# Optimization experiments

Hardware: AMD Instinct MI355X
Metric: run time of the kernel (lower is better)

The kernel has to match this reference:

```python
import jax, jax.numpy as jnp
import numpy as np

B = 256
V = 6890
J = 24
NUM_BETAS = 10
# standard SMPL kinematic tree
PARENTS = np.array([-1, 0, 0, 0, 1, 2, 3, 4, 5, 6, 7, 8, 9, 9, 9, 12, 13, 14, 16, 17, 18, 19, 20, 21], dtype=np.int64)


def setup_inputs() -> dict:
    key = jax.random.key(0)
    ks = jax.random.split(key, 7)
    betas = jax.random.normal(ks[0], (B, NUM_BETAS), dtype=jnp.float32)
    pose = jax.random.normal(ks[1], (B, J * 3), dtype=jnp.float32) * 0.3
    v_template = jax.random.normal(ks[2], (V, 3), dtype=jnp.float32)
    shapedirs = jax.random.normal(ks[3], (V, 3, NUM_BETAS), dtype=jnp.float32) * 0.01
    posedirs = jax.random.normal(ks[4], ((J - 1) * 9, V * 3), dtype=jnp.float32) * 0.01
    jr = jax.random.uniform(ks[5], (J, V), dtype=jnp.float32)
    J_regressor = jr / jnp.sum(jr, axis=1, keepdims=True)
    # skinning weights per vertex sum to 1
    w = jax.random.uniform(ks[6], (V, J), dtype=jnp.float32)
    lbs_weights = w / jnp.sum(w, axis=1, keepdims=True)
    return {"betas": betas, "pose": pose, "v_template": v_template,
            "shapedirs": shapedirs, "posedirs": posedirs,
            "J_regressor": J_regressor, "lbs_weights": lbs_weights,
            "parents": PARENTS}


def batch_rodrigues(rot_vecs):
    # rot_vecs: (N,3) axis-angle -> (N,3,3)
    angle = jnp.linalg.norm(rot_vecs + 1e-8, axis=1, keepdims=True)  # (N,1)
    rot_dir = rot_vecs / angle
    cos = jnp.cos(angle)[:, :, None]  # (N,1,1)
    sin = jnp.sin(angle)[:, :, None]
    rx, ry, rz = rot_dir[:, 0], rot_dir[:, 1], rot_dir[:, 2]
    z = jnp.zeros_like(rx)
    K = jnp.stack([z, -rz, ry, rz, z, -rx, -ry, rx, z], axis=1).reshape(-1, 3, 3)
    ident = jnp.eye(3, dtype=rot_vecs.dtype)[None]
    return ident + sin * K + (1.0 - cos) * jnp.matmul(K, K)


def batch_rigid_transform(rot_mats, joints, parents):
    # rot_mats: (B,J,3,3), joints: (B,J,3)
    b, n = joints.shape[:2]
    rel_joints = joints.at[:, 1:].add(-joints[:, parents[1:]])
    bottom = jnp.broadcast_to(jnp.array([0., 0., 0., 1.], dtype=joints.dtype), (b, n, 1, 4))
    tm = jnp.concatenate([jnp.concatenate([rot_mats, rel_joints[..., None]], axis=-1), bottom], axis=-2)  # (B,J,4,4)
    chain = [tm[:, 0]]
    for i in range(1, n):  # fixed 24-joint kinematic tree
        chain.append(jnp.matmul(chain[int(parents[i])], tm[:, i]))
    transforms = jnp.stack(chain, axis=1)  # (B,J,4,4)
    posed_joints = transforms[:, :, :3, 3]
    joints_homogen = jnp.concatenate([joints, jnp.zeros((b, n, 1), dtype=joints.dtype)], axis=-1)
    t = jnp.einsum('bnij,bnj->bni', transforms, joints_homogen)  # (B,J,4)
    rel_transforms = transforms.at[:, :, :, 3].add(-t)
    return posed_joints, rel_transforms


def reference(betas, pose, v_template, shapedirs, posedirs, J_regressor, lbs_weights, parents):
    b = betas.shape[0]
    ident = jnp.eye(3, dtype=pose.dtype)
    # shape blend shapes
    v_shaped = v_template[None] + jnp.einsum('bl,vkl->bvk', betas, shapedirs)  # (B,V,3)
    Jts = jnp.einsum('bvk,jv->bjk', v_shaped, J_regressor)  # (B,J,3)
    # axis-angle -> rotmats, append 2 identity hand rotations
    rot = batch_rodrigues(pose[:, :-6].reshape(-1, 3)).reshape(b, -1, 3, 3)
    hand = jnp.broadcast_to(ident, (b, 2, 3, 3))
    rot_mats = jnp.concatenate([rot, hand], axis=1)  # (B,24,3,3)
    # pose blend shapes (root excluded)
    pose_feature = (rot_mats[:, 1:] - ident).reshape(b, -1)  # (B,207)
    pose_offsets = jnp.matmul(pose_feature, posedirs).reshape(b, -1, 3)
    v_posed = pose_offsets + v_shaped
    # kinematic chain
    J_transformed, A = batch_rigid_transform(rot_mats, Jts, parents)
    # linear blend skinning
    T = jnp.einsum('vj,bjmn->bvmn', lbs_weights, A)  # (B,V,4,4)
    v_homo = jnp.concatenate([v_posed, jnp.ones((b, v_posed.shape[1], 1), dtype=v_posed.dtype)], axis=-1)
    verts = jnp.einsum('bvmn,bvn->bvm', T, v_homo)[..., :3]
    return verts.astype(jnp.float32), J_transformed.astype(jnp.float32)
```

## Files before the change

kernel.cpp:

```cpp
#include <hip/hip_runtime.h>
#include <math.h>

#define B_N 256
#define V_N 6890
#define J_N 24
#define KPF 207
#define KE  218
#define NCOL (V_N*3)

typedef float v2f __attribute__((ext_vector_type(2)));

__device__ __constant__ int c_par[24] = {-1,0,0,0,1,2,3,4,5,6,7,8,9,9,9,12,13,14,16,17,18,19,20,21};

#define WS_PF   0
#define WS_A    (WS_PF + B_N*KE)
#define WS_EXT  (WS_A + B_N*J_N*12)
#define WS_PART (WS_EXT + 11*NCOL)

__global__ __launch_bounds__(256) void k_jreg(const float* __restrict__ Jreg,
        const float* __restrict__ vt, const float* __restrict__ sd,
        float* __restrict__ part)
{
    int j = blockIdx.x;
    int c = blockIdx.y;
    int tid = threadIdx.x;
    int v0 = c * 1723;
    int v1 = v0 + 1723; if (v1 > V_N) v1 = V_N;

    float acc[33];
    #pragma unroll
    for (int i = 0; i < 33; ++i) acc[i] = 0.f;

    for (int v = v0 + tid; v < v1; v += 256) {
        float r = Jreg[j*V_N + v];
        const float* s = sd + v*30;
        #pragma unroll
        for (int i = 0; i < 30; ++i) acc[i] += r * s[i];
        #pragma unroll
        for (int k = 0; k < 3; ++k) acc[30+k] += r * vt[v*3+k];
    }
    #pragma unroll
    for (int i = 0; i < 33; ++i) {
        #pragma unroll
        for (int off = 32; off > 0; off >>= 1)
            acc[i] += __shfl_down(acc[i], off, 64);
    }
    __shared__ float red[4][33];
    int wave = tid >> 6, lane = tid & 63;
    if (lane == 0) {
        #pragma unroll
        for (int i = 0; i < 33; ++i) red[wave][i] = acc[i];
    }
    __syncthreads();
    if (tid < 33) {
        float s = red[0][tid] + red[1][tid] + red[2][tid] + red[3][tid];
        part[(j*4 + c)*33 + tid] = s;
    }
}

__global__ __launch_bounds__(256) void k_ext(const float* __restrict__ sd,
        const float* __restrict__ vt, float* __restrict__ EXT)
{
    int idx = blockIdx.x*256 + threadIdx.x;
    if (idx >= NCOL) return;
    int v = idx / 3, k = idx - v*3;
    #pragma unroll
    for (int l = 0; l < 10; ++l) EXT[l*NCOL + idx] = sd[v*30 + k*10 + l];
    EXT[10*NCOL + idx] = vt[idx];
}

__global__ __launch_bounds__(64) void k_batch(const float* __restrict__ pose,
        const float* __restrict__ betas, const float* __restrict__ part,
        float* __restrict__ PFt, float* __restrict__ A, float* __restrict__ outJ)
{
    int b = blockIdx.x;
    int lane = threadIdx.x;
    __shared__ float sR[24][9];
    __shared__ float sJ[24][3];
    __shared__ float sG[24][12];

    if (lane < 24) {
        float R[9];
        if (lane < 22) {
            float p0 = pose[b*72 + lane*3 + 0];
            float p1 = pose[b*72 + lane*3 + 1];
            float p2 = pose[b*72 + lane*3 + 2];
            float a0 = p0 + 1e-8f, a1 = p1 + 1e-8f, a2 = p2 + 1e-8f;
            float angle = sqrtf(a0*a0 + a1*a1 + a2*a2);
            float inv = 1.f / angle;
            float rx = p0*inv, ry = p1*inv, rz = p2*inv;
            float cc = cosf(angle), ss = sinf(angle), ic = 1.f - cc;
            R[0] = 1.f - ic*(ry*ry + rz*rz);
            R[1] = -ss*rz + ic*rx*ry;
            R[2] =  ss*ry + ic*rx*rz;
            R[3] =  ss*rz + ic*rx*ry;
            R[4] = 1.f - ic*(rx*rx + rz*rz);
            R[5] = -ss*rx + ic*ry*rz;
            R[6] = -ss*ry + ic*rx*rz;
            R[7] =  ss*rx + ic*ry*rz;
            R[8] = 1.f - ic*(rx*rx + ry*ry);
        } else {
            R[0]=1.f;R[1]=0.f;R[2]=0.f;R[3]=0.f;R[4]=1.f;R[5]=0.f;R[6]=0.f;R[7]=0.f;R[8]=1.f;
        }
        #pragma unroll
        for (int e = 0; e < 9; ++e) sR[lane][e] = R[e];
    }
    __syncthreads();
    for (int idx = lane; idx < 72; idx += 64) {
        int j = idx / 3, k = idx - j*3;
        const float* p0 = part + (j*4 + 0)*33;
        const float* p1 = part + (j*4 + 1)*33;
        const float* p2 = part + (j*4 + 2)*33;
        const float* p3 = part + (j*4 + 3)*33;
        float s = p0[30+k] + p1[30+k] + p2[30+k] + p3[30+k];
        #pragma unroll
        for (int l = 0; l < 10; ++l) {
            float js = p0[k*10+l] + p1[k*10+l] + p2[k*10+l] + p3[k*10+l];
            s += betas[b*10+l] * js;
        }
        sJ[j][k] = s;
    }
    __syncthreads();
    for (int idx = lane; idx < KPF; idx += 64) {
        int jj = 1 + idx/9, e = idx - (idx/9)*9;
        float id = (e==0 || e==4 || e==8) ? 1.f : 0.f;
        PFt[idx*B_N + b] = sR[jj][e] - id;
    }
    if (lane < 10) PFt[(KPF+lane)*B_N + b] = betas[b*10 + lane];
    if (lane == 0) PFt[217*B_N + b] = 1.f;

    if (lane == 0) {
        #pragma unroll
        for (int r = 0; r < 3; ++r) {
            sG[0][r*4+0] = sR[0][r*3+0];
            sG[0][r*4+1] = sR[0][r*3+1];
            sG[0][r*4+2] = sR[0][r*3+2];
            sG[0][r*4+3] = sJ[0][r];
        }
        for (int i = 1; i < 24; ++i) {
            int p = c_par[i];
            float rel0 = sJ[i][0]-sJ[p][0], rel1 = sJ[i][1]-sJ[p][1], rel2 = sJ[i][2]-sJ[p][2];
            for (int r = 0; r < 3; ++r) {
                float g0 = sG[p][r*4+0], g1 = sG[p][r*4+1], g2 = sG[p][r*4+2], g3 = sG[p][r*4+3];
                sG[i][r*4+0] = g0*sR[i][0] + g1*sR[i][3] + g2*sR[i][6];
                sG[i][r*4+1] = g0*sR[i][1] + g1*sR[i][4] + g2*sR[i][7];
                sG[i][r*4+2] = g0*sR[i][2] + g1*sR[i][5] + g2*sR[i][8];
                sG[i][r*4+3] = g0*rel0 + g1*rel1 + g2*rel2 + g3;
            }
        }
    }
    __syncthreads();
    if (lane < 24) {
        int i = lane;
        #pragma unroll
        for (int r = 0; r < 3; ++r) {
            float g0 = sG[i][r*4+0], g1 = sG[i][r*4+1], g2 = sG[i][r*4+2], g3 = sG[i][r*4+3];
            outJ[b*72 + i*3 + r] = g3;
            float t = g3 - (g0*sJ[i][0] + g1*sJ[i][1] + g2*sJ[i][2]);
            A[(b*24+i)*12 + r*4+0] = g0;
            A[(b*24+i)*12 + r*4+1] = g1;
            A[(b*24+i)*12 + r*4+2] = g2;
            A[(b*24+i)*12 + r*4+3] = t;
        }
    }
}

__global__ __launch_bounds__(256, 2) void k_fused(
        const float* __restrict__ posedirs, const float* __restrict__ EXT,
        const float* __restrict__ PFt, const float* __restrict__ A,
        const float* __restrict__ W, float* __restrict__ out)
{
    constexpr int BT = 32;
    __shared__ __align__(16) float smem[BT*288];

    int tid  = threadIdx.x;
    int wave = tid >> 6, lane = tid & 63;

    int bid = blockIdx.x;
    int w   = (bid & 7)*108 + (bid >> 3);
    int vt  = w >> 3, bt = w & 7;
    int v0 = vt * 64;
    int b0 = bt * BT;
    int v  = v0 + lane;

    int col = (v < V_N) ? v*3 : v0*3;

    #pragma unroll 1
    for (int idx = tid; idx < KE*BT; idx += 256) {
        int r = idx >> 5, bl = idx & 31;
        smem[r*BT + bl] = PFt[r*B_N + b0 + bl];
    }
    __syncthreads();

    v2f axy[8];
    v2f az[4];
    #pragma unroll
    for (int k = 0; k < 8; ++k) axy[k] = (v2f){0.f, 0.f};
    #pragma unroll
    for (int k = 0; k < 4; ++k) az[k] = (v2f){0.f, 0.f};

    int pfb = wave*8;

#define ROW_BODY                                                                  \
    {                                                                             \
        float x = p[0], y = p[1], z = p[2];                                       \
        const float4 pa = *reinterpret_cast<const float4*>(&smem[r*BT + pfb]);    \
        const float4 pb = *reinterpret_cast<const float4*>(&smem[r*BT + pfb + 4]);\
        v2f xy = {x, y};                                                          \
        v2f zz = {z, z};                                                          \
        axy[0] = __builtin_elementwise_fma((v2f){pa.x,pa.x}, xy, axy[0]);         \
        axy[1] = __builtin_elementwise_fma((v2f){pa.y,pa.y}, xy, axy[1]);         \
        axy[2] = __builtin_elementwise_fma((v2f){pa.z,pa.z}, xy, axy[2]);         \
        axy[3] = __builtin_elementwise_fma((v2f){pa.w,pa.w}, xy, axy[3]);         \
        axy[4] = __builtin_elementwise_fma((v2f){pb.x,pb.x}, xy, axy[4]);         \
        axy[5] = __builtin_elementwise_fma((v2f){pb.y,pb.y}, xy, axy[5]);         \
        axy[6] = __builtin_elementwise_fma((v2f){pb.z,pb.z}, xy, axy[6]);         \
        axy[7] = __builtin_elementwise_fma((v2f){pb.w,pb.w}, xy, axy[7]);         \
        az[0]  = __builtin_elementwise_fma((v2f){pa.x,pa.y}, zz, az[0]);          \
        az[1]  = __builtin_elementwise_fma((v2f){pa.z,pa.w}, zz, az[1]);          \
        az[2]  = __builtin_elementwise_fma((v2f){pb.x,pb.y}, zz, az[2]);          \
        az[3]  = __builtin_elementwise_fma((v2f){pb.z,pb.w}, zz, az[3]);          \
    }

    {
        const float* p = posedirs + col;
        #pragma unroll 8
        for (int r = 0; r < KPF; ++r) {
            ROW_BODY
            p += NCOL;
        }
    }
    {
        const float* p = EXT + col;
        #pragma unroll
        for (int r = KPF; r < KE; ++r) {
            ROW_BODY
            p += NCOL;
        }
    }
#undef ROW_BODY

    __syncthreads();

    {
        const float* Ag = A + (size_t)b0*288;
        #pragma unroll 1
        for (int idx = tid; idx < BT*288; idx += 256)
            smem[idx] = Ag[idx];
    }

    int vc = (v < V_N) ? v : (V_N - 1);
    const float4* W4 = reinterpret_cast<const float4*>(W + (size_t)vc*24);
    float4 w0 = W4[0], w1 = W4[1], w2 = W4[2], w3 = W4[3], w4 = W4[4], w5 = W4[5];
    __syncthreads();

    float wv[24] = {w0.x,w0.y,w0.z,w0.w, w1.x,w1.y,w1.z,w1.w, w2.x,w2.y,w2.z,w2.w,
                    w3.x,w3.y,w3.z,w3.w, w4.x,w4.y,w4.z,w4.w, w5.x,w5.y,w5.z,w5.w};

    #pragma unroll
    for (int k = 0; k < 8; ++k) {
        int bb = wave*8 + k;
        const float* Ab = smem + bb*288;
        v2f T01 = {0.f,0.f}, T23 = {0.f,0.f}, T45 = {0.f,0.f};
        v2f T67 = {0.f,0.f}, T89 = {0.f,0.f}, Tab = {0.f,0.f};
        #pragma unroll
        for (int j = 0; j < 24; ++j) {
            float ww = wv[j];
            v2f wwv = {ww, ww};
            float4 a0 = *reinterpret_cast<const float4*>(Ab + j*12 + 0);
            float4 a1 = *reinterpret_cast<const float4*>(Ab + j*12 + 4);
            float4 a2 = *reinterpret_cast<const float4*>(Ab + j*12 + 8);
            T01 = __builtin_elementwise_fma(wwv, (v2f){a0.x,a0.y}, T01);
            T23 = __builtin_elementwise_fma(wwv, (v2f){a0.z,a0.w}, T23);
            T45 = __builtin_elementwise_fma(wwv, (v2f){a1.x,a1.y}, T45);
            T67 = __builtin_elementwise_fma(wwv, (v2f){a1.z,a1.w}, T67);
            T89 = __builtin_elementwise_fma(wwv, (v2f){a2.x,a2.y}, T89);
            Tab = __builtin_elementwise_fma(wwv, (v2f){a2.z,a2.w}, Tab);
        }
        if (v < V_N) {
            float x = axy[k].x, y = axy[k].y;
            float z = (k & 1) ? az[k>>1].y : az[k>>1].x;
            size_t o = (size_t)(b0 + bb)*NCOL + (size_t)v*3;
            out[o+0] = T01.x*x + T01.y*y + T23.x*z + T23.y;
            out[o+1] = T45.x*x + T45.y*y + T67.x*z + T67.y;
            out[o+2] = T89.x*x + T89.y*y + Tab.x*z + Tab.y;
        }
    }
}

extern "C" void kernel_launch(void* const* d_in, const int* in_sizes, int n_in,
                              void* d_out, int out_size, void* d_ws, size_t ws_size,
                              hipStream_t stream)
{
    const float* betas      = (const float*)d_in[0];
    const float* pose       = (const float*)d_in[1];
    const float* v_template = (const float*)d_in[2];
    const float* shapedirs  = (const float*)d_in[3];
    const float* posedirs   = (const float*)d_in[4];
    const float* Jreg       = (const float*)d_in[5];
    const float* lbs        = (const float*)d_in[6];

    float* ws   = (float*)d_ws;
    float* PFt  = ws + WS_PF;
    float* A    = ws + WS_A;
    float* EXT  = ws + WS_EXT;
    float* part = ws + WS_PART;

    float* verts = (float*)d_out;
    float* outJ  = verts + (size_t)B_N*V_N*3;

    hipLaunchKernelGGL(k_jreg, dim3(24,4), dim3(256), 0, stream, Jreg, v_template, shapedirs, part);
    hipLaunchKernelGGL(k_ext, dim3((NCOL+255)/256), dim3(256), 0, stream, shapedirs, v_template, EXT);
    hipLaunchKernelGGL(k_batch, dim3(256), dim3(64), 0, stream, pose, betas, part, PFt, A, outJ);
    hipLaunchKernelGGL(k_fused, dim3(8*108), dim3(256), 0, stream, posedirs, EXT, PFt, A, lbs, verts);
}
```

Baseline: 87.41 us.

## Merge preprocessing kernels and halve shared memory in fused skinning kernel

```diff
diff --git a/kernel.cpp b/kernel.cpp
--- a/kernel.cpp
+++ b/kernel.cpp
@@ -17,56 +17,57 @@
 #define WS_EXT  (WS_A + B_N*J_N*12)
 #define WS_PART (WS_EXT + 11*NCOL)
 
-__global__ __launch_bounds__(256) void k_jreg(const float* __restrict__ Jreg,
+__global__ __launch_bounds__(256) void k_pre(const float* __restrict__ Jreg,
         const float* __restrict__ vt, const float* __restrict__ sd,
-        float* __restrict__ part)
+        float* __restrict__ part, float* __restrict__ EXT)
 {
-    int j = blockIdx.x;
-    int c = blockIdx.y;
+    int bid = blockIdx.x;
     int tid = threadIdx.x;
-    int v0 = c * 1723;
-    int v1 = v0 + 1723; if (v1 > V_N) v1 = V_N;
-
-    float acc[33];
-    #pragma unroll
-    for (int i = 0; i < 33; ++i) acc[i] = 0.f;
-
-    for (int v = v0 + tid; v < v1; v += 256) {
-        float r = Jreg[j*V_N + v];
-        const float* s = sd + v*30;
-        #pragma unroll
-        for (int i = 0; i < 30; ++i) acc[i] += r * s[i];
-        #pragma unroll
-        for (int k = 0; k < 3; ++k) acc[30+k] += r * vt[v*3+k];
-    }
-    #pragma unroll
-    for (int i = 0; i < 33; ++i) {
-        #pragma unroll
-        for (int off = 32; off > 0; off >>= 1)
-            acc[i] += __shfl_down(acc[i], off, 64);
-    }
     __shared__ float red[4][33];
-    int wave = tid >> 6, lane = tid & 63;
-    if (lane == 0) {
-        #pragma unroll
-        for (int i = 0; i < 33; ++i) red[wave][i] = acc[i];
-    }
-    __syncthreads();
-    if (tid < 33) {
-        float s = red[0][tid] + red[1][tid] + red[2][tid] + red[3][tid];
-        part[(j*4 + c)*33 + tid] = s;
-    }
-}
-
-__global__ __launch_bounds__(256) void k_ext(const float* __restrict__ sd,
-        const float* __restrict__ vt, float* __restrict__ EXT)
-{
-    int idx = blockIdx.x*256 + threadIdx.x;
-    if (idx >= NCOL) return;
-    int v = idx / 3, k = idx - v*3;
-    #pragma unroll
-    for (int l = 0; l < 10; ++l) EXT[l*NCOL + idx] = sd[v*30 + k*10 + l];
-    EXT[10*NCOL + idx] = vt[idx];
+
+    if (bid < 96) {
+        int j = bid >> 2;
+        int c = bid & 3;
+        int v0 = c * 1723;
+        int v1 = v0 + 1723; if (v1 > V_N) v1 = V_N;
+
+        float acc[33];
+        #pragma unroll
+        for (int i = 0; i < 33; ++i) acc[i] = 0.f;
+
+        for (int v = v0 + tid; v < v1; v += 256) {
+            float r = Jreg[j*V_N + v];
+            const float* s = sd + v*30;
+            #pragma unroll
+            for (int i = 0; i < 30; ++i) acc[i] += r * s[i];
+            #pragma unroll
+            for (int k = 0; k < 3; ++k) acc[30+k] += r * vt[v*3+k];
+        }
+        #pragma unroll
+        for (int i = 0; i < 33; ++i) {
+            #pragma unroll
+            for (int off = 32; off > 0; off >>= 1)
+                acc[i] += __shfl_down(acc[i], off, 64);
+        }
+        int wave = tid >> 6, lane = tid & 63;
+        if (lane == 0) {
+            #pragma unroll
+            for (int i = 0; i < 33; ++i) red[wave][i] = acc[i];
+        }
+        __syncthreads();
+        if (tid < 33) {
+            float s = red[0][tid] + red[1][tid] + red[2][tid] + red[3][tid];
+            part[(j*4 + c)*33 + tid] = s;
+        }
+    } else {
+        int idx = (bid - 96)*256 + tid;
+        if (idx < NCOL) {
+            int v = idx / 3, k = idx - v*3;
+            #pragma unroll
+            for (int l = 0; l < 10; ++l) EXT[l*NCOL + idx] = sd[v*30 + k*10 + l];
+            EXT[10*NCOL + idx] = vt[idx];
+        }
+    }
 }
 
 __global__ __launch_bounds__(64) void k_batch(const float* __restrict__ pose,
@@ -171,7 +172,7 @@
         const float* __restrict__ W, float* __restrict__ out)
 {
     constexpr int BT = 32;
-    __shared__ __align__(16) float smem[BT*288];
+    __shared__ __align__(16) float smem[KE*BT];
 
     int tid  = threadIdx.x;
     int wave = tid >> 6, lane = tid & 63;
@@ -199,13 +200,14 @@
     #pragma unroll
     for (int k = 0; k < 4; ++k) az[k] = (v2f){0.f, 0.f};
 
-    int pfb = wave*8;
+    int pfa = wave*4;
+    int pfb = 16 + wave*4;
 
 #define ROW_BODY                                                                  \
     {                                                                             \
         float x = p[0], y = p[1], z = p[2];                                       \
-        const float4 pa = *reinterpret_cast<const float4*>(&smem[r*BT + pfb]);    \
-        const float4 pb = *reinterpret_cast<const float4*>(&smem[r*BT + pfb + 4]);\
+        const float4 pa = *reinterpret_cast<const float4*>(&smem[r*BT + pfa]);    \
+        const float4 pb = *reinterpret_cast<const float4*>(&smem[r*BT + pfb]);    \
         v2f xy = {x, y};                                                          \
         v2f zz = {z, z};                                                          \
         axy[0] = __builtin_elementwise_fma((v2f){pa.x,pa.x}, xy, axy[0]);         \
@@ -240,50 +242,52 @@
     }
 #undef ROW_BODY
 
-    __syncthreads();
-
-    {
-        const float* Ag = A + (size_t)b0*288;
-        #pragma unroll 1
-        for (int idx = tid; idx < BT*288; idx += 256)
-            smem[idx] = Ag[idx];
-    }
-
     int vc = (v < V_N) ? v : (V_N - 1);
     const float4* W4 = reinterpret_cast<const float4*>(W + (size_t)vc*24);
     float4 w0 = W4[0], w1 = W4[1], w2 = W4[2], w3 = W4[3], w4 = W4[4], w5 = W4[5];
-    __syncthreads();
-
     float wv[24] = {w0.x,w0.y,w0.z,w0.w, w1.x,w1.y,w1.z,w1.w, w2.x,w2.y,w2.z,w2.w,
                     w3.x,w3.y,w3.z,w3.w, w4.x,w4.y,w4.z,w4.w, w5.x,w5.y,w5.z,w5.w};
 
-    #pragma unroll
-    for (int k = 0; k < 8; ++k) {
-        int bb = wave*8 + k;
-        const float* Ab = smem + bb*288;
-        v2f T01 = {0.f,0.f}, T23 = {0.f,0.f}, T45 = {0.f,0.f};
-        v2f T67 = {0.f,0.f}, T89 = {0.f,0.f}, Tab = {0.f,0.f};
-        #pragma unroll
-        for (int j = 0; j < 24; ++j) {
-            float ww = wv[j];
-            v2f wwv = {ww, ww};
-            float4 a0 = *reinterpret_cast<const float4*>(Ab + j*12 + 0);
-            float4 a1 = *reinterpret_cast<const float4*>(Ab + j*12 + 4);
-            float4 a2 = *reinterpret_cast<const float4*>(Ab + j*12 + 8);
-            T01 = __builtin_elementwise_fma(wwv, (v2f){a0.x,a0.y}, T01);
-            T23 = __builtin_elementwise_fma(wwv, (v2f){a0.z,a0.w}, T23);
-            T45 = __builtin_elementwise_fma(wwv, (v2f){a1.x,a1.y}, T45);
-            T67 = __builtin_elementwise_fma(wwv, (v2f){a1.z,a1.w}, T67);
-            T89 = __builtin_elementwise_fma(wwv, (v2f){a2.x,a2.y}, T89);
-            Tab = __builtin_elementwise_fma(wwv, (v2f){a2.z,a2.w}, Tab);
-        }
-        if (v < V_N) {
-            float x = axy[k].x, y = axy[k].y;
-            float z = (k & 1) ? az[k>>1].y : az[k>>1].x;
-            size_t o = (size_t)(b0 + bb)*NCOL + (size_t)v*3;
-            out[o+0] = T01.x*x + T01.y*y + T23.x*z + T23.y;
-            out[o+1] = T45.x*x + T45.y*y + T67.x*z + T67.y;
-            out[o+2] = T89.x*x + T89.y*y + Tab.x*z + Tab.y;
+    #pragma unroll 1
+    for (int h = 0; h < 2; ++h) {
+        __syncthreads();
+        {
+            const float* Ag = A + (size_t)(b0 + h*16)*288;
+            #pragma unroll 1
+            for (int idx = tid; idx < 16*288; idx += 256)
+                smem[idx] = Ag[idx];
+        }
+        __syncthreads();
+
+        #pragma unroll
+        for (int q = 0; q < 4; ++q) {
+            int k   = h*4 + q;
+            int bbl = h*16 + wave*4 + q;
+            const float* Ab = smem + (wave*4 + q)*288;
+            v2f T01 = {0.f,0.f}, T23 = {0.f,0.f}, T45 = {0.f,0.f};
+            v2f T67 = {0.f,0.f}, T89 = {0.f,0.f}, Tab = {0.f,0.f};
+            #pragma unroll
+            for (int j = 0; j < 24; ++j) {
+                float ww = wv[j];
+                v2f wwv = {ww, ww};
+                float4 a0 = *reinterpret_cast<const float4*>(Ab + j*12 + 0);
+                float4 a1 = *reinterpret_cast<const float4*>(Ab + j*12 + 4);
+                float4 a2 = *reinterpret_cast<const float4*>(Ab + j*12 + 8);
+                T01 = __builtin_elementwise_fma(wwv, (v2f){a0.x,a0.y}, T01);
+                T23 = __builtin_elementwise_fma(wwv, (v2f){a0.z,a0.w}, T23);
+                T45 = __builtin_elementwise_fma(wwv, (v2f){a1.x,a1.y}, T45);
+                T67 = __builtin_elementwise_fma(wwv, (v2f){a1.z,a1.w}, T67);
+                T89 = __builtin_elementwise_fma(wwv, (v2f){a2.x,a2.y}, T89);
+                Tab = __builtin_elementwise_fma(wwv, (v2f){a2.z,a2.w}, Tab);
+            }
+            if (v < V_N) {
+                float x = axy[k].x, y = axy[k].y;
+                float z = (k & 1) ? az[k>>1].y : az[k>>1].x;
+                size_t o = (size_t)(b0 + bbl)*NCOL + (size_t)v*3;
+                out[o+0] = T01.x*x + T01.y*y + T23.x*z + T23.y;
+                out[o+1] = T45.x*x + T45.y*y + T67.x*z + T67.y;
+                out[o+2] = T89.x*x + T89.y*y + Tab.x*z + Tab.y;
+            }
         }
     }
 }
@@ -309,8 +313,7 @@
     float* verts = (float*)d_out;
     float* outJ  = verts + (size_t)B_N*V_N*3;
 
-    hipLaunchKernelGGL(k_jreg, dim3(24,4), dim3(256), 0, stream, Jreg, v_template, shapedirs, part);
-    hipLaunchKernelGGL(k_ext, dim3((NCOL+255)/256), dim3(256), 0, stream, shapedirs, v_template, EXT);
+    hipLaunchKernelGGL(k_pre, dim3(96 + 81), dim3(256), 0, stream, Jreg, v_template, shapedirs, part, EXT);
     hipLaunchKernelGGL(k_batch, dim3(256), dim3(64), 0, stream, pose, betas, part, PFt, A, outJ);
     hipLaunchKernelGGL(k_fused, dim3(8*108), dim3(256), 0, stream, posedirs, EXT, PFt, A, lbs, verts);
 }
```

New measurement: 106.0 us. 21.3% more time.
